# Kernel optimization log

Hardware: AMD Instinct MI355X
Metric: run time of the kernel (lower is better)

## Reference

```python
import jax, jax.numpy as jnp
import numpy as np

N, B, L, C, H = 16384, 16, 32, 256, 8
DH = C // H
K_STATIC = 16   # k_max for L=32 (L>20 -> min(16, L//2))
K_MIN = 8       # int(0.25*L)
LN_EPS = 1e-5


def _ln(x, g, b):
    m = x.mean(-1, keepdims=True)
    v = ((x - m) ** 2).mean(-1, keepdims=True)
    return (x - m) / jnp.sqrt(v + LN_EPS) * g + b


def setup_inputs() -> dict:
    key = jax.random.key(0)
    ks = jax.random.split(key, 12)
    s = 1.0 / np.sqrt(C)
    f32 = jnp.float32
    return {
        'vision_features': jax.random.normal(ks[0], (N, B, C), dtype=f32),
        'text_features': jax.random.normal(ks[1], (L, B, C), dtype=f32),
        'vp_w': jax.random.normal(ks[2], (C, C), dtype=f32) * s,
        'vp_b': jnp.zeros((C,), f32),
        'tp_w': jax.random.normal(ks[3], (C, C), dtype=f32) * s,
        'tp_b': jnp.zeros((C,), f32),
        'in_proj_w': jax.random.normal(ks[4], (3 * C, C), dtype=f32) * s,
        'in_proj_b': jnp.zeros((3 * C,), f32),
        'w1': jax.random.normal(ks[5], (C, C), dtype=f32) * s,
        'b1': jnp.zeros((C,), f32),
        'g1': jnp.ones((C,), f32),
        'be1': jnp.zeros((C,), f32),
        'w2': jax.random.normal(ks[6], (C // 2, C), dtype=f32) * s,
        'b2': jnp.zeros((C // 2,), f32),
        'g2': jnp.ones((C // 2,), f32),
        'be2': jnp.zeros((C // 2,), f32),
        'w3': jax.random.normal(ks[7], (1, C // 2), dtype=f32) * s,
        'b3': jnp.zeros((1,), f32),
        'k_weight': jnp.asarray(np.log(0.4 / 0.6), f32),
        'alpha_coarse': jnp.asarray(np.log(0.72 / 0.28), f32),
        'alpha_fine': jnp.asarray(np.log(0.82 / 0.18), f32),
    }


def reference(vision_features, text_features, vp_w, vp_b, tp_w, tp_b,
              in_proj_w, in_proj_b, w1, b1, g1, be1, w2, b2, g2, be2,
              w3, b3, k_weight, alpha_coarse, alpha_fine):
    # projections (torch Linear: y = x W^T + b)
    vision_proj = vision_features @ vp_w.T + vp_b  # [N,B,C]
    text_proj = text_features @ tp_w.T + tp_b      # [L,B,C]

    # nn.MultiheadAttention attention weights, averaged over heads
    qp = vision_proj @ in_proj_w[:C].T + in_proj_b[:C]
    kp = text_proj @ in_proj_w[C:2 * C].T + in_proj_b[C:2 * C]
    q = qp.reshape(N, B, H, DH)
    k = kp.reshape(L, B, H, DH)
    scores = jnp.einsum('nbhd,lbhd->bhnl', q, k) / np.sqrt(DH)
    attn = jax.nn.softmax(scores, axis=-1).mean(axis=1)  # [B,N,L]

    # data-dependent k_top per batch (unbiased variance over L, mean over N)
    mu = attn.mean(axis=-1, keepdims=True)
    var = ((attn - mu) ** 2).sum(axis=-1) / (L - 1)       # [B,N]
    attn_variance = var.mean(axis=1)                      # [B]
    k_ws = jax.nn.sigmoid(k_weight)
    ratio = jnp.clip(k_ws * (1.0 + attn_variance * 0.5), 0.25, 0.6)
    k_base = jnp.maximum(1, jnp.floor(L * ratio).astype(jnp.int32))
    k_top = jnp.maximum(K_MIN, jnp.minimum(jnp.minimum(K_STATIC, k_base), L))  # [B]

    # variable-k top-k via static K_STATIC + mask
    top = -jnp.sort(-attn, axis=-1)[..., :K_STATIC]       # [B,N,K]
    mask = jnp.arange(K_STATIC)[None, None, :] < k_top[:, None, None]
    logits = jnp.where(mask, top, -jnp.inf)
    w = jax.nn.softmax(logits, axis=-1)
    similarity_score = jnp.sum(jnp.where(mask, top * w, 0.0), axis=-1)  # [B,N]

    # importance MLP on raw vision features (dropout off at inference)
    h = jax.nn.relu(_ln(vision_features @ w1.T + b1, g1, be1))
    h = jax.nn.relu(_ln(h @ w2.T + b2, g2, be2))
    feature_importance = jax.nn.sigmoid(h @ w3.T + b3)[..., 0]  # [N,B]
    feature_importance = feature_importance.T                    # [B,N]

    def minmax(x):
        lo = x.min(axis=1, keepdims=True)
        rng = x.max(axis=1, keepdims=True) - lo
        return jnp.where(rng > 0, (x - lo) / rng, 0.0)

    sim_norm = minmax(similarity_score)
    imp_norm = minmax(feature_importance)

    alpha = (jax.nn.sigmoid(alpha_coarse) + jax.nn.sigmoid(alpha_fine)) / 2.0
    importance = alpha * sim_norm + (1.0 - alpha) * imp_norm  # [B,N]
    return importance.T  # [N,B]
```

## Files before the change

kernel.cpp:

```cpp
#include <hip/hip_runtime.h>
#include <hip/hip_bf16.h>

typedef _Float16 f16;
typedef _Float16 half8 __attribute__((ext_vector_type(8)));
typedef _Float16 half4 __attribute__((ext_vector_type(4)));
typedef float f32x4 __attribute__((ext_vector_type(4)));

typedef const __attribute__((address_space(1))) void gvoid;
typedef __attribute__((address_space(3))) void lvoid;
#define GLOAD16(src, dst) __builtin_amdgcn_global_load_lds((gvoid*)(src), (lvoid*)(dst), 16, 0, 0)

#define WQV_OFF   0u
#define WKT_OFF   262144u
#define KP_OFF    524288u
#define W2S_OFF   1048576u
#define SBIAS_OFF 3145728u
#define BQV_OFF   3162112u
#define BKT_OFF   3163136u
#define W1H_OFF   3164160u
#define W2H_OFF   3295232u
#define VARP_OFF  3360768u
#define SMM_OFF   3377280u
#define FMM_OFF   3377408u
#define CAND_OFF  3377664u
#define FI_OFF    12814848u
#define SIM_OFF   13863424u

__device__ __forceinline__ float sigm(float x) { return 1.f / (1.f + __expf(-x)); }
__device__ __forceinline__ unsigned fmap(float f) {
  unsigned u = __float_as_uint(f);
  return (u & 0x80000000u) ? ~u : (u | 0x80000000u);
}
__device__ __forceinline__ float funmap(unsigned u) {
  unsigned b = (u & 0x80000000u) ? (u & 0x7FFFFFFFu) : ~u;
  return __uint_as_float(b);
}
__device__ __forceinline__ unsigned fragoff(int o, int c) {
  int ot = o >> 4, ln = o & 15;
  int kc = c >> 6, mi = (c >> 5) & 1, kg = (c >> 3) & 3, h8 = c & 7;
  return (unsigned)((((ot * 4 + kc) * 2 + mi) << 10) + ((kg * 16 + ln) << 4) + h8 * 2);
}

__global__ void k_p1(const float* __restrict__ ipw, const float* __restrict__ ipb,
                     const float* __restrict__ vp_w, const float* __restrict__ vp_b,
                     const float* __restrict__ tp_w, const float* __restrict__ tp_b,
                     float* __restrict__ Wqv, float* __restrict__ Wkt,
                     float* __restrict__ bqv, float* __restrict__ bkt,
                     unsigned* __restrict__ simMM, unsigned* __restrict__ fiMM) {
  int tx = threadIdx.x, ty = threadIdx.y;
  int bz = blockIdx.z;
  if (bz == 2) {
    if (blockIdx.x || blockIdx.y) return;
    if (ty == 0 && tx < 16) {
      simMM[tx * 2] = 0xFFFFFFFFu; simMM[tx * 2 + 1] = 0u;
      fiMM[tx * 2] = 0xFFFFFFFFu;  fiMM[tx * 2 + 1] = 0u;
    }
    int j = ty * 16 + tx;
    float s1 = 0.f, s2 = 0.f;
    for (int k = 0; k < 256; ++k) {
      s1 += ipw[j * 256 + k] * vp_b[k];
      s2 += ipw[65536 + j * 256 + k] * tp_b[k];
    }
    bqv[j] = s1 + ipb[j];
    bkt[j] = s2 + ipb[256 + j];
    return;
  }
  const float* A = ipw + (bz ? 65536 : 0);
  const float* B = bz ? tp_w : vp_w;
  float* O = bz ? Wkt : Wqv;
  __shared__ float As[16][16], Bs[16][17];
  int row = blockIdx.y * 16 + ty, col = blockIdx.x * 16 + tx;
  float s = 0.f;
  for (int tt = 0; tt < 16; ++tt) {
    As[ty][tx] = A[row * 256 + tt * 16 + tx];
    Bs[ty][tx] = B[(tt * 16 + ty) * 256 + col];
    __syncthreads();
#pragma unroll
    for (int k = 0; k < 16; ++k) s += As[ty][k] * Bs[k][tx];
    __syncthreads();
  }
  O[row * 256 + col] = s;
}

__global__ void k_conv(const float* __restrict__ w1, const float* __restrict__ w2,
                       char* __restrict__ W1g, char* __restrict__ W2g) {
  int i = blockIdx.x * 256 + threadIdx.x;
  if (i < 65536) {
    int o = i >> 8, c = i & 255;
    *(f16*)(W1g + (c >> 6) * 32768 + o * 128 + (((c & 63) << 1) ^ ((o & 7) << 4))) = (f16)w1[i];
  } else if (i < 98304) {
    int i2 = i - 65536;
    int o = i2 >> 8, c = i2 & 255;
    *(f16*)(W2g + fragoff(o, c)) = (f16)w2[i2];
  }
}

__global__ void k_p2(const float* __restrict__ T, const float* __restrict__ Wkt,
                     const float* __restrict__ bkt, float* __restrict__ kp) {
  __shared__ float As[16][16], Ws[16][17];
  int tx = threadIdx.x, ty = threadIdx.y;
  int lb = blockIdx.y * 16 + ty;
  int i = blockIdx.x * 16 + tx;
  float s = 0.f;
  for (int tt = 0; tt < 16; ++tt) {
    As[ty][tx] = T[(size_t)lb * 256 + tt * 16 + tx];
    Ws[ty][tx] = Wkt[(size_t)(blockIdx.x * 16 + ty) * 256 + tt * 16 + tx];
    __syncthreads();
#pragma unroll
    for (int k = 0; k < 16; ++k) s += As[ty][k] * Ws[tx][k];
    __syncthreads();
  }
  kp[(size_t)lb * 256 + i] = s + bkt[i];
}

__global__ void k_p3(const float* __restrict__ kp, const float* __restrict__ Wqv,
                     const float* __restrict__ bqv, char* __restrict__ W2sg,
                     float* __restrict__ sbias) {
  const float SC = 0.17677669529663687f;
  int b = blockIdx.z, jt = blockIdx.y, ct = blockIdx.x;
  int ty = threadIdx.y, tx = threadIdx.x;
  int j2 = jt * 16 + ty, c = ct * 16 + tx;
  int h = j2 >> 5, l = j2 & 31;
  const float* kr = kp + (size_t)(l * 16 + b) * 256 + h * 32;
  const float* wq = Wqv + (size_t)h * 32 * 256 + c;
  float s = 0.f;
#pragma unroll
  for (int d = 0; d < 32; ++d) s += kr[d] * wq[(size_t)d * 256];
  *(f16*)(W2sg + (size_t)b * 131072 + (c >> 6) * 32768 + j2 * 128 +
          (((c & 63) << 1) ^ ((j2 & 7) << 4))) = (f16)(s * SC);
  if (ct == 0 && tx == 0) {
    float sb = 0.f;
#pragma unroll
    for (int d = 0; d < 32; ++d) sb += kr[d] * bqv[h * 32 + d];
    sbias[b * 256 + j2] = sb * SC;
  }
}

__global__ void __launch_bounds__(256, 4) k_main(
    const float* __restrict__ X, const char* __restrict__ W2sg,
    const float* __restrict__ sbias,
    const char* __restrict__ W1g, const char* __restrict__ W2g,
    const float* __restrict__ b1, const float* __restrict__ g1, const float* __restrict__ be1,
    const float* __restrict__ b2, const float* __restrict__ g2, const float* __restrict__ be2,
    const float* __restrict__ w3, const float* __restrict__ b3,
    float* __restrict__ cand, float* __restrict__ varpart, float* __restrict__ fi) {
  __shared__ __align__(16) char smem[40960];
  const int b = blockIdx.y;
  const int bx = blockIdx.x;
  const int n0 = bx * 64;
  const int t = threadIdx.x;
  const int w = t >> 6;
  const int lane = t & 63;
  const int ln = lane & 15, kg = lane >> 4;
  char* AT = smem;
  char* BT = smem + 8192;

  auto issueA = [&](int kt) {
    int row = t >> 2, cq = t & 3;
    const float* Xr = X + ((size_t)(n0 + row) * 16 + b) * 256 + kt * 64 + cq * 16;
    f32x4 a0 = *(const f32x4*)(Xr), a1 = *(const f32x4*)(Xr + 4);
    f32x4 a2 = *(const f32x4*)(Xr + 8), a3 = *(const f32x4*)(Xr + 12);
    half8 h0, h1;
#pragma unroll
    for (int i = 0; i < 4; ++i) {
      h0[i] = (f16)a0[i]; h0[4 + i] = (f16)a1[i];
      h1[i] = (f16)a2[i]; h1[4 + i] = (f16)a3[i];
    }
    unsigned sw = (unsigned)((row & 7) << 4);
    *(half8*)(AT + ((unsigned)(row * 128 + cq * 32) ^ sw)) = h0;
    *(half8*)(AT + ((unsigned)(row * 128 + cq * 32 + 16) ^ sw)) = h1;
  };

  if (blockIdx.z == 0) {
    const char* Wb = W2sg + (size_t)b * 131072;
    auto issueB = [&](int kt) {
      const char* src = Wb + kt * 32768 + w * 8192 + (lane << 4);
      char* dst = BT + w * 8192;
#pragma unroll
      for (int i = 0; i < 8; ++i) GLOAD16(src + i * 1024, dst + i * 1024);
    };

    f32x4 acc[4][4];
#pragma unroll
    for (int q = 0; q < 4; ++q)
#pragma unroll
      for (int ni = 0; ni < 4; ++ni)
#pragma unroll
        for (int i = 0; i < 4; ++i) acc[q][ni][i] = 0.f;

    issueA(0); issueB(0);
    __syncthreads();
#pragma unroll
    for (int kt = 0; kt < 4; ++kt) {
      half8 av[4][2], bv[4][2];
#pragma unroll
      for (int q = 0; q < 4; ++q) {
        int o = w * 64 + q * 16 + ln;
        unsigned sw = (unsigned)((o & 7) << 4);
#pragma unroll
        for (int mi = 0; mi < 2; ++mi)
          av[q][mi] = *(const half8*)(BT + o * 128 + ((unsigned)(mi * 64 + kg * 16) ^ sw));
      }
#pragma unroll
      for (int ni = 0; ni < 4; ++ni) {
        int n = ni * 16 + ln;
        unsigned sw = (unsigned)((n & 7) << 4);
#pragma unroll
        for (int mi = 0; mi < 2; ++mi)
          bv[ni][mi] = *(const half8*)(AT + n * 128 + ((unsigned)(mi * 64 + kg * 16) ^ sw));
      }
#pragma unroll
      for (int mi = 0; mi < 2; ++mi)
#pragma unroll
        for (int q = 0; q < 4; ++q)
#pragma unroll
          for (int ni = 0; ni < 4; ++ni)
            acc[q][ni] = __builtin_amdgcn_mfma_f32_16x16x32_f16(av[q][mi], bv[ni][mi], acc[q][ni], 0, 0, 0);
      __syncthreads();
      if (kt < 3) { issueA(kt + 1); issueB(kt + 1); __syncthreads(); }
    }

    {
      f32x4 sb[4];
#pragma unroll
      for (int q = 0; q < 4; ++q)
        sb[q] = *(const f32x4*)(sbias + b * 256 + (w * 4 + q) * 16 + kg * 4);
      float vm[4][2][4];
#pragma unroll
      for (int ni = 0; ni < 4; ++ni)
#pragma unroll
        for (int qq = 0; qq < 2; ++qq)
#pragma unroll
          for (int r = 0; r < 4; ++r) vm[ni][qq][r] = 0.f;
#pragma unroll
      for (int hh = 0; hh < 2; ++hh)
#pragma unroll
        for (int ni = 0; ni < 4; ++ni) {
          float x[2][4];
          float mx = -1e30f;
#pragma unroll
          for (int qq = 0; qq < 2; ++qq)
#pragma unroll
            for (int r = 0; r < 4; ++r) {
              x[qq][r] = acc[hh * 2 + qq][ni][r] + sb[hh * 2 + qq][r];
              mx = fmaxf(mx, x[qq][r]);
            }
          mx = fmaxf(mx, __shfl_xor(mx, 16, 64));
          mx = fmaxf(mx, __shfl_xor(mx, 32, 64));
          float S = 0.f;
#pragma unroll
          for (int qq = 0; qq < 2; ++qq)
#pragma unroll
            for (int r = 0; r < 4; ++r) { x[qq][r] = __expf(x[qq][r] - mx); S += x[qq][r]; }
          S += __shfl_xor(S, 16, 64);
          S += __shfl_xor(S, 32, 64);
          float inv = 0.125f / S;
#pragma unroll
          for (int qq = 0; qq < 2; ++qq)
#pragma unroll
            for (int r = 0; r < 4; ++r) vm[ni][qq][r] += x[qq][r] * inv;
        }
      float* slice = (float*)(smem + 8192) + w * 2048;
#pragma unroll
      for (int ni = 0; ni < 4; ++ni)
#pragma unroll
        for (int qq = 0; qq < 2; ++qq)
#pragma unroll
          for (int r = 0; r < 4; ++r)
            slice[(qq * 16 + kg * 4 + r) * 64 + ni * 16 + ln] = vm[ni][qq][r];
    }
    __syncthreads();

    if (w == 0) {
      const float* sl = (const float*)(smem + 8192);
      float v[32];
#pragma unroll
      for (int l = 0; l < 32; ++l)
        v[l] = sl[l * 64 + lane] + sl[2048 + l * 64 + lane] +
               sl[4096 + l * 64 + lane] + sl[6144 + l * 64 + lane];
      float s2 = 0.f;
#pragma unroll
      for (int l = 0; l < 32; ++l) s2 += v[l] * v[l];
      float vr = (s2 - (1.f / 32.f)) * (1.f / 31.f);
#pragma unroll
      for (int m = 1; m < 64; m <<= 1) vr += __shfl_xor(vr, m, 64);
      if (lane == 0) varpart[b * 256 + bx] = vr;
#pragma unroll
      for (int k = 2; k <= 32; k <<= 1) {
#pragma unroll
        for (int j = k >> 1; j > 0; j >>= 1) {
#pragma unroll
          for (int i = 0; i < 32; ++i) {
            int l = i ^ j;
            if (l > i) {
              float a = v[i], c = v[l];
              float hi = fmaxf(a, c), lo = fminf(a, c);
              bool up = ((i & k) == 0);
              v[i] = up ? hi : lo;
              v[l] = up ? lo : hi;
            }
          }
        }
      }
      float m0 = v[0], se = 0.f, te = 0.f;
      float cn[9];
#pragma unroll
      for (int i = 0; i < 16; ++i) {
        float e = __expf(v[i] - m0);
        se += e; te += v[i] * e;
        if (i >= 7) cn[i - 7] = te / se;
      }
#pragma unroll
      for (int i = 0; i < 9; ++i)
        cand[(size_t)i * 262144 + (size_t)b * 16384 + n0 + lane] = cn[i];
    }
    return;
  }

  char* H1 = smem;
  float* pS = (float*)(smem + 32768);
  float* pQ = (float*)(smem + 34048);
  float* pM = (float*)(smem + 35328);
  float* pR = (float*)(smem + 35584);
  auto issueB1 = [&](int kt) {
    const char* src = W1g + kt * 32768 + w * 8192 + (lane << 4);
    char* dst = BT + w * 8192;
#pragma unroll
    for (int i = 0; i < 8; ++i) GLOAD16(src + i * 1024, dst + i * 1024);
  };

  f32x4 acc[4][4];
#pragma unroll
  for (int q = 0; q < 4; ++q)
#pragma unroll
    for (int ni = 0; ni < 4; ++ni)
#pragma unroll
      for (int i = 0; i < 4; ++i) acc[q][ni][i] = 0.f;

  issueA(0); issueB1(0);
  __syncthreads();
#pragma unroll
  for (int kt = 0; kt < 4; ++kt) {
    half8 av[4][2], bv[4][2];
#pragma unroll
    for (int q = 0; q < 4; ++q) {
      int o = w * 64 + q * 16 + ln;
      unsigned sw = (unsigned)((o & 7) << 4);
#pragma unroll
      for (int mi = 0; mi < 2; ++mi)
        av[q][mi] = *(const half8*)(BT + o * 128 + ((unsigned)(mi * 64 + kg * 16) ^ sw));
    }
#pragma unroll
    for (int ni = 0; ni < 4; ++ni) {
      int n = ni * 16 + ln;
      unsigned sw = (unsigned)((n & 7) << 4);
#pragma unroll
      for (int mi = 0; mi < 2; ++mi)
        bv[ni][mi] = *(const half8*)(AT + n * 128 + ((unsigned)(mi * 64 + kg * 16) ^ sw));
    }
#pragma unroll
    for (int mi = 0; mi < 2; ++mi)
#pragma unroll
      for (int q = 0; q < 4; ++q)
#pragma unroll
        for (int ni = 0; ni < 4; ++ni)
          acc[q][ni] = __builtin_amdgcn_mfma_f32_16x16x32_f16(av[q][mi], bv[ni][mi], acc[q][ni], 0, 0, 0);
    __syncthreads();
    if (kt < 3) { issueA(kt + 1); issueB1(kt + 1); __syncthreads(); }
  }

  {
    f32x4 b1v[4];
#pragma unroll
    for (int q = 0; q < 4; ++q)
      b1v[q] = *(const f32x4*)(b1 + (w * 4 + q) * 16 + kg * 4);
#pragma unroll
    for (int ni = 0; ni < 4; ++ni) {
      float s = 0.f, qq = 0.f;
#pragma unroll
      for (int q = 0; q < 4; ++q)
#pragma unroll
        for (int r = 0; r < 4; ++r) {
          float v = acc[q][ni][r] + b1v[q][r];
          acc[q][ni][r] = v;
          s += v; qq += v * v;
        }
      s += __shfl_xor(s, 16, 64); s += __shfl_xor(s, 32, 64);
      qq += __shfl_xor(qq, 16, 64); qq += __shfl_xor(qq, 32, 64);
      if (kg == 0) { int n = ni * 16 + ln; pS[n * 5 + w] = s; pQ[n * 5 + w] = qq; }
    }
  }
  __syncthreads();
  if (t < 64) {
    float s = pS[t * 5 + 0] + pS[t * 5 + 1] + pS[t * 5 + 2] + pS[t * 5 + 3];
    float q = pQ[t * 5 + 0] + pQ[t * 5 + 1] + pQ[t * 5 + 2] + pQ[t * 5 + 3];
    float mean = s * (1.f / 256.f);
    float var = q * (1.f / 256.f) - mean * mean;
    pM[t] = mean;
    pR[t] = rsqrtf(var + 1e-5f);
  }
  __syncthreads();

  {
    f32x4 g1v[4], e1v[4];
#pragma unroll
    for (int q = 0; q < 4; ++q) {
      g1v[q] = *(const f32x4*)(g1 + (w * 4 + q) * 16 + kg * 4);
      e1v[q] = *(const f32x4*)(be1 + (w * 4 + q) * 16 + kg * 4);
    }
#pragma unroll
    for (int ni = 0; ni < 4; ++ni) {
      int n = ni * 16 + ln;
      float mean = pM[n], rstd = pR[n];
      unsigned sw = (unsigned)((n & 7) << 4);
#pragma unroll
      for (int q = 0; q < 4; ++q) {
        half4 hv;
#pragma unroll
        for (int r = 0; r < 4; ++r) {
          float y = (acc[q][ni][r] - mean) * rstd * g1v[q][r] + e1v[q][r];
          hv[r] = (f16)fmaxf(y, 0.f);
        }
        *(half4*)(H1 + ((unsigned)(n * 512 + (w * 4 + q) * 32 + kg * 8) ^ sw)) = hv;
      }
    }
  }
  __syncthreads();

  f32x4 acc2[2][4];
#pragma unroll
  for (int oi = 0; oi < 2; ++oi)
#pragma unroll
    for (int ni = 0; ni < 4; ++ni)
#pragma unroll
      for (int i = 0; i < 4; ++i) acc2[oi][ni][i] = 0.f;
#pragma unroll
  for (int kt = 0; kt < 4; ++kt) {
    half8 a2[2][2], bv[4][2];
#pragma unroll
    for (int oi = 0; oi < 2; ++oi)
#pragma unroll
      for (int mi = 0; mi < 2; ++mi)
        a2[oi][mi] = *(const half8*)(W2g + ((((w * 2 + oi) * 4 + kt) * 2 + mi) << 10) + (lane << 4));
#pragma unroll
    for (int ni = 0; ni < 4; ++ni) {
      int n = ni * 16 + ln;
      unsigned sw = (unsigned)((n & 7) << 4);
#pragma unroll
      for (int mi = 0; mi < 2; ++mi)
        bv[ni][mi] = *(const half8*)(H1 + n * 512 + kt * 128 + ((unsigned)(mi * 64 + kg * 16) ^ sw));
    }
#pragma unroll
    for (int mi = 0; mi < 2; ++mi)
#pragma unroll
      for (int oi = 0; oi < 2; ++oi)
#pragma unroll
        for (int ni = 0; ni < 4; ++ni)
          acc2[oi][ni] = __builtin_amdgcn_mfma_f32_16x16x32_f16(a2[oi][mi], bv[ni][mi], acc2[oi][ni], 0, 0, 0);
  }

  {
    f32x4 b2v[2], g2v[2], e2v[2], w3v[2];
#pragma unroll
    for (int oi = 0; oi < 2; ++oi) {
      b2v[oi] = *(const f32x4*)(b2 + (w * 2 + oi) * 16 + kg * 4);
      g2v[oi] = *(const f32x4*)(g2 + (w * 2 + oi) * 16 + kg * 4);
      e2v[oi] = *(const f32x4*)(be2 + (w * 2 + oi) * 16 + kg * 4);
      w3v[oi] = *(const f32x4*)(w3 + (w * 2 + oi) * 16 + kg * 4);
    }
    __syncthreads();
#pragma unroll
    for (int ni = 0; ni < 4; ++ni) {
      float s = 0.f, q = 0.f;
#pragma unroll
      for (int oi = 0; oi < 2; ++oi)
#pragma unroll
        for (int r = 0; r < 4; ++r) {
          float v = acc2[oi][ni][r] + b2v[oi][r];
          acc2[oi][ni][r] = v;
          s += v; q += v * v;
        }
      s += __shfl_xor(s, 16, 64); s += __shfl_xor(s, 32, 64);
      q += __shfl_xor(q, 16, 64); q += __shfl_xor(q, 32, 64);
      if (kg == 0) { int n = ni * 16 + ln; pS[n * 5 + w] = s; pQ[n * 5 + w] = q; }
    }
    __syncthreads();
    if (t < 64) {
      float s = pS[t * 5 + 0] + pS[t * 5 + 1] + pS[t * 5 + 2] + pS[t * 5 + 3];
      float q = pQ[t * 5 + 0] + pQ[t * 5 + 1] + pQ[t * 5 + 2] + pQ[t * 5 + 3];
      float mean = s * (1.f / 128.f);
      float var = q * (1.f / 128.f) - mean * mean;
      pM[t] = mean;
      pR[t] = rsqrtf(var + 1e-5f);
    }
    __syncthreads();
#pragma unroll
    for (int ni = 0; ni < 4; ++ni) {
      int n = ni * 16 + ln;
      float mean = pM[n], rstd = pR[n];
      float a3 = 0.f;
#pragma unroll
      for (int oi = 0; oi < 2; ++oi)
#pragma unroll
        for (int r = 0; r < 4; ++r) {
          float y = (acc2[oi][ni][r] - mean) * rstd * g2v[oi][r] + e2v[oi][r];
          a3 += fmaxf(y, 0.f) * w3v[oi][r];
        }
      a3 += __shfl_xor(a3, 16, 64);
      a3 += __shfl_xor(a3, 32, 64);
      if (kg == 0) pS[n * 5 + w] = a3;
    }
    __syncthreads();
    if (t < 64) {
      float z = pS[t * 5 + 0] + pS[t * 5 + 1] + pS[t * 5 + 2] + pS[t * 5 + 3] + b3[0];
      fi[(size_t)b * 16384 + n0 + t] = sigm(z);
    }
  }
}

__global__ void __launch_bounds__(256) k_g4(
    const float* __restrict__ cand, const float* __restrict__ fi,
    const float* __restrict__ varpart, const float* __restrict__ kw,
    float* __restrict__ sim, unsigned* __restrict__ simMM, unsigned* __restrict__ fiMM) {
  __shared__ float red[4][4];
  __shared__ int kS;
  int b = blockIdx.x >> 6;
  if (threadIdx.x < 64) {
    float s = 0.f;
#pragma unroll
    for (int i = 0; i < 4; ++i) s += varpart[b * 256 + threadIdx.x + i * 64];
#pragma unroll
    for (int m = 1; m < 64; m <<= 1) s += __shfl_xor(s, m, 64);
    if (threadIdx.x == 0) {
      float var = s * (1.f / 16384.f);
      float kws = sigm(kw[0]);
      float ratio = fminf(fmaxf(kws * (1.f + var * 0.5f), 0.25f), 0.6f);
      int kb = (int)floorf(32.f * ratio);
      if (kb < 1) kb = 1;
      int kt = kb < 16 ? kb : 16;
      if (kt < 8) kt = 8;
      kS = kt;
    }
  }
  __syncthreads();
  int k = kS;
  int n = (blockIdx.x & 63) * 256 + threadIdx.x;
  size_t idx = (size_t)b * 16384 + n;
  float sv = cand[(size_t)(k - 8) * 262144 + idx];
  sim[idx] = sv;
  float fv = fi[idx];
  float sn = sv, sx = sv, fn = fv, fx = fv;
#pragma unroll
  for (int m = 1; m < 64; m <<= 1) {
    sn = fminf(sn, __shfl_xor(sn, m, 64));
    sx = fmaxf(sx, __shfl_xor(sx, m, 64));
    fn = fminf(fn, __shfl_xor(fn, m, 64));
    fx = fmaxf(fx, __shfl_xor(fx, m, 64));
  }
  int wv = threadIdx.x >> 6;
  if ((threadIdx.x & 63) == 0) { red[0][wv] = sn; red[1][wv] = sx; red[2][wv] = fn; red[3][wv] = fx; }
  __syncthreads();
  if (threadIdx.x == 0) {
    float a = red[0][0], c = red[1][0], d = red[2][0], e = red[3][0];
#pragma unroll
    for (int i = 1; i < 4; ++i) {
      a = fminf(a, red[0][i]); c = fmaxf(c, red[1][i]);
      d = fminf(d, red[2][i]); e = fmaxf(e, red[3][i]);
    }
    atomicMin(&simMM[b * 2 + 0], fmap(a));
    atomicMax(&simMM[b * 2 + 1], fmap(c));
    atomicMin(&fiMM[b * 2 + 0], fmap(d));
    atomicMax(&fiMM[b * 2 + 1], fmap(e));
  }
}

__global__ void __launch_bounds__(256) k_g5(
    const float* __restrict__ sim, const float* __restrict__ fi,
    const unsigned* __restrict__ simMM, const unsigned* __restrict__ fiMM,
    const float* __restrict__ ac, const float* __restrict__ af,
    float* __restrict__ out) {
  __shared__ float ls[256][17], lf[256][17];
  __shared__ float sMin[16], sInv[16], fMin[16], fInv[16];
  int t = threadIdx.x;
  int n0 = blockIdx.x * 256;
  if (t < 16) {
    float lo = funmap(simMM[t * 2]), hi = funmap(simMM[t * 2 + 1]);
    float r = hi - lo;
    sMin[t] = lo; sInv[t] = (r > 0.f) ? 1.f / r : 0.f;
    lo = funmap(fiMM[t * 2]); hi = funmap(fiMM[t * 2 + 1]);
    r = hi - lo;
    fMin[t] = lo; fInv[t] = (r > 0.f) ? 1.f / r : 0.f;
  }
#pragma unroll
  for (int i = 0; i < 16; ++i) {
    ls[t][i] = sim[(size_t)i * 16384 + n0 + t];
    lf[t][i] = fi[(size_t)i * 16384 + n0 + t];
  }
  __syncthreads();
  float alpha = 0.5f * (sigm(ac[0]) + sigm(af[0]));
  float o[16];
#pragma unroll
  for (int b = 0; b < 16; ++b) {
    float s = (ls[t][b] - sMin[b]) * sInv[b];
    float f = (lf[t][b] - fMin[b]) * fInv[b];
    o[b] = alpha * s + (1.f - alpha) * f;
  }
  float* op = out + (size_t)(n0 + t) * 16;
#pragma unroll
  for (int i = 0; i < 4; ++i) {
    f32x4 v;
    v[0] = o[i * 4]; v[1] = o[i * 4 + 1]; v[2] = o[i * 4 + 2]; v[3] = o[i * 4 + 3];
    *(f32x4*)(op + i * 4) = v;
  }
}

extern "C" void kernel_launch(void* const* d_in, const int* in_sizes, int n_in,
                              void* d_out, int out_size, void* d_ws, size_t ws_size,
                              hipStream_t stream) {
  const float* X    = (const float*)d_in[0];
  const float* T    = (const float*)d_in[1];
  const float* vp_w = (const float*)d_in[2];
  const float* vp_b = (const float*)d_in[3];
  const float* tp_w = (const float*)d_in[4];
  const float* tp_b = (const float*)d_in[5];
  const float* ipw  = (const float*)d_in[6];
  const float* ipb  = (const float*)d_in[7];
  const float* w1   = (const float*)d_in[8];
  const float* b1   = (const float*)d_in[9];
  const float* g1   = (const float*)d_in[10];
  const float* be1  = (const float*)d_in[11];
  const float* w2   = (const float*)d_in[12];
  const float* b2   = (const float*)d_in[13];
  const float* g2   = (const float*)d_in[14];
  const float* be2  = (const float*)d_in[15];
  const float* w3   = (const float*)d_in[16];
  const float* b3   = (const float*)d_in[17];
  const float* kw   = (const float*)d_in[18];
  const float* ac   = (const float*)d_in[19];
  const float* af   = (const float*)d_in[20];
  char* ws = (char*)d_ws;
  float* Wqv = (float*)(ws + WQV_OFF);
  float* Wkt = (float*)(ws + WKT_OFF);
  float* kp = (float*)(ws + KP_OFF);
  char* W2sg = ws + W2S_OFF;
  float* sbias = (float*)(ws + SBIAS_OFF);
  float* bqv = (float*)(ws + BQV_OFF);
  float* bkt = (float*)(ws + BKT_OFF);
  char* W1g = ws + W1H_OFF;
  char* W2g = ws + W2H_OFF;
  float* varpart = (float*)(ws + VARP_OFF);
  unsigned* simMM = (unsigned*)(ws + SMM_OFF);
  unsigned* fiMM = (unsigned*)(ws + FMM_OFF);
  float* cand = (float*)(ws + CAND_OFF);
  float* fi = (float*)(ws + FI_OFF);
  float* sim = (float*)(ws + SIM_OFF);
  float* out = (float*)d_out;

  k_p1<<<dim3(16, 16, 3), dim3(16, 16), 0, stream>>>(ipw, ipb, vp_w, vp_b, tp_w, tp_b,
                                                     Wqv, Wkt, bqv, bkt, simMM, fiMM);
  k_conv<<<384, 256, 0, stream>>>(w1, w2, W1g, W2g);
  k_p2<<<dim3(16, 32), dim3(16, 16), 0, stream>>>(T, Wkt, bkt, kp);
  k_p3<<<dim3(16, 16, 16), dim3(16, 16), 0, stream>>>(kp, Wqv, bqv, W2sg, sbias);
  k_main<<<dim3(256, 16, 2), 256, 0, stream>>>(X, W2sg, sbias, W1g, W2g,
                                               b1, g1, be1, b2, g2, be2, w3, b3,
                                               cand, varpart, fi);
  k_g4<<<1024, 256, 0, stream>>>(cand, fi, varpart, kw, sim, simMM, fiMM);
  k_g5<<<64, 256, 0, stream>>>(sim, fi, simMM, fiMM, ac, af, out);
}
```

Baseline: 257.4 us.

## Merge attention and MLP branches of k_main to share one staged X tile

The two blockIdx.z branches of k_main, which each loaded and converted the same 64-row X tile, become one block that stages the full fp16 X tile in shared memory once. The block then runs the attention-score GEMM and the importance-MLP GEMM in sequence, reusing both the X tile and the weight buffer, and writes the first-layer activations back over the X region. This halves the global X reads and the f32-to-f16 conversion work. In exchange, shared memory grows to about 67KB, launch bounds drop to 2 blocks per SM, and each block does serial work with less parallelism across blocks.

```diff
diff --git a/kernel.cpp b/kernel.cpp
--- a/kernel.cpp
+++ b/kernel.cpp
@@ -136,7 +136,7 @@
   }
 }
 
-__global__ void __launch_bounds__(256, 4) k_main(
+__global__ void __launch_bounds__(256, 2) k_main(
     const float* __restrict__ X, const char* __restrict__ W2sg,
     const float* __restrict__ sbias,
     const char* __restrict__ W1g, const char* __restrict__ W2g,
@@ -144,7 +144,7 @@
     const float* __restrict__ b2, const float* __restrict__ g2, const float* __restrict__ be2,
     const float* __restrict__ w3, const float* __restrict__ b3,
     float* __restrict__ cand, float* __restrict__ varpart, float* __restrict__ fi) {
-  __shared__ __align__(16) char smem[40960];
+  __shared__ __align__(16) char smem[68608];
   const int b = blockIdx.y;
   const int bx = blockIdx.x;
   const int n0 = bx * 64;
@@ -152,221 +152,192 @@
   const int w = t >> 6;
   const int lane = t & 63;
   const int ln = lane & 15, kg = lane >> 4;
-  char* AT = smem;
-  char* BT = smem + 8192;
-
-  auto issueA = [&](int kt) {
+  char* XT = smem;
+  char* WB = smem + 32768;
+  float* pS = (float*)(smem + 65536);
+  float* pQ = (float*)(smem + 66816);
+  float* pM = (float*)(smem + 68096);
+  float* pR = (float*)(smem + 68352);
+
+  {
     int row = t >> 2, cq = t & 3;
-    const float* Xr = X + ((size_t)(n0 + row) * 16 + b) * 256 + kt * 64 + cq * 16;
-    f32x4 a0 = *(const f32x4*)(Xr), a1 = *(const f32x4*)(Xr + 4);
-    f32x4 a2 = *(const f32x4*)(Xr + 8), a3 = *(const f32x4*)(Xr + 12);
-    half8 h0, h1;
-#pragma unroll
-    for (int i = 0; i < 4; ++i) {
-      h0[i] = (f16)a0[i]; h0[4 + i] = (f16)a1[i];
-      h1[i] = (f16)a2[i]; h1[4 + i] = (f16)a3[i];
-    }
+    const float* Xr = X + ((size_t)(n0 + row) * 16 + b) * 256;
     unsigned sw = (unsigned)((row & 7) << 4);
-    *(half8*)(AT + ((unsigned)(row * 128 + cq * 32) ^ sw)) = h0;
-    *(half8*)(AT + ((unsigned)(row * 128 + cq * 32 + 16) ^ sw)) = h1;
+#pragma unroll
+    for (int kt = 0; kt < 4; ++kt) {
+      f32x4 a0 = *(const f32x4*)(Xr + kt * 64 + cq * 16);
+      f32x4 a1 = *(const f32x4*)(Xr + kt * 64 + cq * 16 + 4);
+      f32x4 a2 = *(const f32x4*)(Xr + kt * 64 + cq * 16 + 8);
+      f32x4 a3 = *(const f32x4*)(Xr + kt * 64 + cq * 16 + 12);
+      half8 h0, h1;
+#pragma unroll
+      for (int i = 0; i < 4; ++i) {
+        h0[i] = (f16)a0[i]; h0[4 + i] = (f16)a1[i];
+        h1[i] = (f16)a2[i]; h1[4 + i] = (f16)a3[i];
+      }
+      unsigned base = (unsigned)(row * 512 + kt * 128 + cq * 32);
+      *(half8*)(XT + ((base) ^ sw)) = h0;
+      *(half8*)(XT + ((base + 16) ^ sw)) = h1;
+    }
+  }
+
+  auto issueW = [&](const char* Wimg, int kt) {
+    const char* src = Wimg + kt * 32768 + w * 8192 + (lane << 4);
+    char* dst = WB + w * 8192;
+#pragma unroll
+    for (int i = 0; i < 8; ++i) GLOAD16(src + i * 1024, dst + i * 1024);
   };
 
-  if (blockIdx.z == 0) {
-    const char* Wb = W2sg + (size_t)b * 131072;
-    auto issueB = [&](int kt) {
-      const char* src = Wb + kt * 32768 + w * 8192 + (lane << 4);
-      char* dst = BT + w * 8192;
-#pragma unroll
-      for (int i = 0; i < 8; ++i) GLOAD16(src + i * 1024, dst + i * 1024);
-    };
-
-    f32x4 acc[4][4];
+  f32x4 acc[4][4];
+  auto zeroAcc = [&]() {
 #pragma unroll
     for (int q = 0; q < 4; ++q)
 #pragma unroll
       for (int ni = 0; ni < 4; ++ni)
 #pragma unroll
         for (int i = 0; i < 4; ++i) acc[q][ni][i] = 0.f;
-
-    issueA(0); issueB(0);
-    __syncthreads();
-#pragma unroll
-    for (int kt = 0; kt < 4; ++kt) {
-      half8 av[4][2], bv[4][2];
-#pragma unroll
-      for (int q = 0; q < 4; ++q) {
-        int o = w * 64 + q * 16 + ln;
-        unsigned sw = (unsigned)((o & 7) << 4);
-#pragma unroll
-        for (int mi = 0; mi < 2; ++mi)
-          av[q][mi] = *(const half8*)(BT + o * 128 + ((unsigned)(mi * 64 + kg * 16) ^ sw));
+  };
+  auto gemm_kt = [&](int kt) {
+    half8 av[4][2], bv[4][2];
+#pragma unroll
+    for (int q = 0; q < 4; ++q) {
+      int o = w * 64 + q * 16 + ln;
+      unsigned sw = (unsigned)((o & 7) << 4);
+#pragma unroll
+      for (int mi = 0; mi < 2; ++mi)
+        av[q][mi] = *(const half8*)(WB + o * 128 + ((unsigned)(mi * 64 + kg * 16) ^ sw));
+    }
+#pragma unroll
+    for (int ni = 0; ni < 4; ++ni) {
+      int n = ni * 16 + ln;
+      unsigned sw = (unsigned)((n & 7) << 4);
+#pragma unroll
+      for (int mi = 0; mi < 2; ++mi)
+        bv[ni][mi] = *(const half8*)(XT + n * 512 + kt * 128 + ((unsigned)(mi * 64 + kg * 16) ^ sw));
+    }
+#pragma unroll
+    for (int mi = 0; mi < 2; ++mi)
+#pragma unroll
+      for (int q = 0; q < 4; ++q)
+#pragma unroll
+        for (int ni = 0; ni < 4; ++ni)
+          acc[q][ni] = __builtin_amdgcn_mfma_f32_16x16x32_f16(av[q][mi], bv[ni][mi], acc[q][ni], 0, 0, 0);
+  };
+
+  zeroAcc();
+  issueW(W2sg + (size_t)b * 131072, 0);
+  __syncthreads();
+#pragma unroll
+  for (int kt = 0; kt < 4; ++kt) {
+    gemm_kt(kt);
+    __syncthreads();
+    if (kt < 3) { issueW(W2sg + (size_t)b * 131072, kt + 1); __syncthreads(); }
+  }
+
+  {
+    f32x4 sb[4];
+#pragma unroll
+    for (int q = 0; q < 4; ++q)
+      sb[q] = *(const f32x4*)(sbias + b * 256 + (w * 4 + q) * 16 + kg * 4);
+    float vm[4][2][4];
+#pragma unroll
+    for (int ni = 0; ni < 4; ++ni)
+#pragma unroll
+      for (int qq = 0; qq < 2; ++qq)
+#pragma unroll
+        for (int r = 0; r < 4; ++r) vm[ni][qq][r] = 0.f;
+#pragma unroll
+    for (int hh = 0; hh < 2; ++hh)
+#pragma unroll
+      for (int ni = 0; ni < 4; ++ni) {
+        float x[2][4];
+        float mx = -1e30f;
+#pragma unroll
+        for (int qq = 0; qq < 2; ++qq)
+#pragma unroll
+          for (int r = 0; r < 4; ++r) {
+            x[qq][r] = acc[hh * 2 + qq][ni][r] + sb[hh * 2 + qq][r];
+            mx = fmaxf(mx, x[qq][r]);
+          }
+        mx = fmaxf(mx, __shfl_xor(mx, 16, 64));
+        mx = fmaxf(mx, __shfl_xor(mx, 32, 64));
+        float S = 0.f;
+#pragma unroll
+        for (int qq = 0; qq < 2; ++qq)
+#pragma unroll
+          for (int r = 0; r < 4; ++r) { x[qq][r] = __expf(x[qq][r] - mx); S += x[qq][r]; }
+        S += __shfl_xor(S, 16, 64);
+        S += __shfl_xor(S, 32, 64);
+        float inv = 0.125f / S;
+#pragma unroll
+        for (int qq = 0; qq < 2; ++qq)
+#pragma unroll
+          for (int r = 0; r < 4; ++r) vm[ni][qq][r] += x[qq][r] * inv;
       }
-#pragma unroll
-      for (int ni = 0; ni < 4; ++ni) {
-        int n = ni * 16 + ln;
-        unsigned sw = (unsigned)((n & 7) << 4);
-#pragma unroll
-        for (int mi = 0; mi < 2; ++mi)
-          bv[ni][mi] = *(const half8*)(AT + n * 128 + ((unsigned)(mi * 64 + kg * 16) ^ sw));
-      }
-#pragma unroll
-      for (int mi = 0; mi < 2; ++mi)
-#pragma unroll
-        for (int q = 0; q < 4; ++q)
-#pragma unroll
-          for (int ni = 0; ni < 4; ++ni)
-            acc[q][ni] = __builtin_amdgcn_mfma_f32_16x16x32_f16(av[q][mi], bv[ni][mi], acc[q][ni], 0, 0, 0);
-      __syncthreads();
-      if (kt < 3) { issueA(kt + 1); issueB(kt + 1); __syncthreads(); }
-    }
-
-    {
-      f32x4 sb[4];
-#pragma unroll
-      for (int q = 0; q < 4; ++q)
-        sb[q] = *(const f32x4*)(sbias + b * 256 + (w * 4 + q) * 16 + kg * 4);
-      float vm[4][2][4];
-#pragma unroll
-      for (int ni = 0; ni < 4; ++ni)
-#pragma unroll
-        for (int qq = 0; qq < 2; ++qq)
-#pragma unroll
-          for (int r = 0; r < 4; ++r) vm[ni][qq][r] = 0.f;
-#pragma unroll
-      for (int hh = 0; hh < 2; ++hh)
-#pragma unroll
-        for (int ni = 0; ni < 4; ++ni) {
-          float x[2][4];
-          float mx = -1e30f;
-#pragma unroll
-          for (int qq = 0; qq < 2; ++qq)
-#pragma unroll
-            for (int r = 0; r < 4; ++r) {
-              x[qq][r] = acc[hh * 2 + qq][ni][r] + sb[hh * 2 + qq][r];
-              mx = fmaxf(mx, x[qq][r]);
-            }
-          mx = fmaxf(mx, __shfl_xor(mx, 16, 64));
-          mx = fmaxf(mx, __shfl_xor(mx, 32, 64));
-          float S = 0.f;
-#pragma unroll
-          for (int qq = 0; qq < 2; ++qq)
-#pragma unroll
-            for (int r = 0; r < 4; ++r) { x[qq][r] = __expf(x[qq][r] - mx); S += x[qq][r]; }
-          S += __shfl_xor(S, 16, 64);
-          S += __shfl_xor(S, 32, 64);
-          float inv = 0.125f / S;
-#pragma unroll
-          for (int qq = 0; qq < 2; ++qq)
-#pragma unroll
-            for (int r = 0; r < 4; ++r) vm[ni][qq][r] += x[qq][r] * inv;
-        }
-      float* slice = (float*)(smem + 8192) + w * 2048;
-#pragma unroll
-      for (int ni = 0; ni < 4; ++ni)
-#pragma unroll
-        for (int qq = 0; qq < 2; ++qq)
-#pragma unroll
-          for (int r = 0; r < 4; ++r)
-            slice[(qq * 16 + kg * 4 + r) * 64 + ni * 16 + ln] = vm[ni][qq][r];
-    }
-    __syncthreads();
-
-    if (w == 0) {
-      const float* sl = (const float*)(smem + 8192);
-      float v[32];
-#pragma unroll
-      for (int l = 0; l < 32; ++l)
-        v[l] = sl[l * 64 + lane] + sl[2048 + l * 64 + lane] +
-               sl[4096 + l * 64 + lane] + sl[6144 + l * 64 + lane];
-      float s2 = 0.f;
-#pragma unroll
-      for (int l = 0; l < 32; ++l) s2 += v[l] * v[l];
-      float vr = (s2 - (1.f / 32.f)) * (1.f / 31.f);
-#pragma unroll
-      for (int m = 1; m < 64; m <<= 1) vr += __shfl_xor(vr, m, 64);
-      if (lane == 0) varpart[b * 256 + bx] = vr;
-#pragma unroll
-      for (int k = 2; k <= 32; k <<= 1) {
-#pragma unroll
-        for (int j = k >> 1; j > 0; j >>= 1) {
-#pragma unroll
-          for (int i = 0; i < 32; ++i) {
-            int l = i ^ j;
-            if (l > i) {
-              float a = v[i], c = v[l];
-              float hi = fmaxf(a, c), lo = fminf(a, c);
-              bool up = ((i & k) == 0);
-              v[i] = up ? hi : lo;
-              v[l] = up ? lo : hi;
-            }
+    float* slice = (float*)WB + w * 2048;
+#pragma unroll
+    for (int ni = 0; ni < 4; ++ni)
+#pragma unroll
+      for (int qq = 0; qq < 2; ++qq)
+#pragma unroll
+        for (int r = 0; r < 4; ++r)
+          slice[(qq * 16 + kg * 4 + r) * 64 + ni * 16 + ln] = vm[ni][qq][r];
+  }
+  __syncthreads();
+
+  if (w == 0) {
+    const float* sl = (const float*)WB;
+    float v[32];
+#pragma unroll
+    for (int l = 0; l < 32; ++l)
+      v[l] = sl[l * 64 + lane] + sl[2048 + l * 64 + lane] +
+             sl[4096 + l * 64 + lane] + sl[6144 + l * 64 + lane];
+    float s2 = 0.f;
+#pragma unroll
+    for (int l = 0; l < 32; ++l) s2 += v[l] * v[l];
+    float vr = (s2 - (1.f / 32.f)) * (1.f / 31.f);
+#pragma unroll
+    for (int m = 1; m < 64; m <<= 1) vr += __shfl_xor(vr, m, 64);
+    if (lane == 0) varpart[b * 256 + bx] = vr;
+#pragma unroll
+    for (int k = 2; k <= 32; k <<= 1) {
+#pragma unroll
+      for (int j = k >> 1; j > 0; j >>= 1) {
+#pragma unroll
+        for (int i = 0; i < 32; ++i) {
+          int l = i ^ j;
+          if (l > i) {
+            float a = v[i], c = v[l];
+            float hi = fmaxf(a, c), lo = fminf(a, c);
+            bool up = ((i & k) == 0);
+            v[i] = up ? hi : lo;
+            v[l] = up ? lo : hi;
           }
         }
       }
-      float m0 = v[0], se = 0.f, te = 0.f;
-      float cn[9];
-#pragma unroll
-      for (int i = 0; i < 16; ++i) {
-        float e = __expf(v[i] - m0);
-        se += e; te += v[i] * e;
-        if (i >= 7) cn[i - 7] = te / se;
-      }
-#pragma unroll
-      for (int i = 0; i < 9; ++i)
-        cand[(size_t)i * 262144 + (size_t)b * 16384 + n0 + lane] = cn[i];
-    }
-    return;
-  }
-
-  char* H1 = smem;
-  float* pS = (float*)(smem + 32768);
-  float* pQ = (float*)(smem + 34048);
-  float* pM = (float*)(smem + 35328);
-  float* pR = (float*)(smem + 35584);
-  auto issueB1 = [&](int kt) {
-    const char* src = W1g + kt * 32768 + w * 8192 + (lane << 4);
-    char* dst = BT + w * 8192;
-#pragma unroll
-    for (int i = 0; i < 8; ++i) GLOAD16(src + i * 1024, dst + i * 1024);
-  };
-
-  f32x4 acc[4][4];
-#pragma unroll
-  for (int q = 0; q < 4; ++q)
-#pragma unroll
-    for (int ni = 0; ni < 4; ++ni)
-#pragma unroll
-      for (int i = 0; i < 4; ++i) acc[q][ni][i] = 0.f;
-
-  issueA(0); issueB1(0);
+    }
+    float m0 = v[0], se = 0.f, te = 0.f;
+    float cn[9];
+#pragma unroll
+    for (int i = 0; i < 16; ++i) {
+      float e = __expf(v[i] - m0);
+      se += e; te += v[i] * e;
+      if (i >= 7) cn[i - 7] = te / se;
+    }
+#pragma unroll
+    for (int i = 0; i < 9; ++i)
+      cand[(size_t)i * 262144 + (size_t)b * 16384 + n0 + lane] = cn[i];
+  }
+  __syncthreads();
+
+  zeroAcc();
+  issueW(W1g, 0);
   __syncthreads();
 #pragma unroll
   for (int kt = 0; kt < 4; ++kt) {
-    half8 av[4][2], bv[4][2];
-#pragma unroll
-    for (int q = 0; q < 4; ++q) {
-      int o = w * 64 + q * 16 + ln;
-      unsigned sw = (unsigned)((o & 7) << 4);
-#pragma unroll
-      for (int mi = 0; mi < 2; ++mi)
-        av[q][mi] = *(const half8*)(BT + o * 128 + ((unsigned)(mi * 64 + kg * 16) ^ sw));
-    }
-#pragma unroll
-    for (int ni = 0; ni < 4; ++ni) {
-      int n = ni * 16 + ln;
-      unsigned sw = (unsigned)((n & 7) << 4);
-#pragma unroll
-      for (int mi = 0; mi < 2; ++mi)
-        bv[ni][mi] = *(const half8*)(AT + n * 128 + ((unsigned)(mi * 64 + kg * 16) ^ sw));
-    }
-#pragma unroll
-    for (int mi = 0; mi < 2; ++mi)
-#pragma unroll
-      for (int q = 0; q < 4; ++q)
-#pragma unroll
-        for (int ni = 0; ni < 4; ++ni)
-          acc[q][ni] = __builtin_amdgcn_mfma_f32_16x16x32_f16(av[q][mi], bv[ni][mi], acc[q][ni], 0, 0, 0);
-    __syncthreads();
-    if (kt < 3) { issueA(kt + 1); issueB1(kt + 1); __syncthreads(); }
+    gemm_kt(kt);
+    __syncthreads();
+    if (kt < 3) { issueW(W1g, kt + 1); __syncthreads(); }
   }
 
   {
@@ -421,7 +392,7 @@
           float y = (acc[q][ni][r] - mean) * rstd * g1v[q][r] + e1v[q][r];
           hv[r] = (f16)fmaxf(y, 0.f);
         }
-        *(half4*)(H1 + ((unsigned)(n * 512 + (w * 4 + q) * 32 + kg * 8) ^ sw)) = hv;
+        *(half4*)(XT + ((unsigned)(n * 512 + (w * 4 + q) * 32 + kg * 8) ^ sw)) = hv;
       }
     }
   }
@@ -448,7 +419,7 @@
       unsigned sw = (unsigned)((n & 7) << 4);
 #pragma unroll
       for (int mi = 0; mi < 2; ++mi)
-        bv[ni][mi] = *(const half8*)(H1 + n * 512 + kt * 128 + ((unsigned)(mi * 64 + kg * 16) ^ sw));
+        bv[ni][mi] = *(const half8*)(XT + n * 512 + kt * 128 + ((unsigned)(mi * 64 + kg * 16) ^ sw));
     }
 #pragma unroll
     for (int mi = 0; mi < 2; ++mi)
@@ -661,9 +632,9 @@
   k_conv<<<384, 256, 0, stream>>>(w1, w2, W1g, W2g);
   k_p2<<<dim3(16, 32), dim3(16, 16), 0, stream>>>(T, Wkt, bkt, kp);
   k_p3<<<dim3(16, 16, 16), dim3(16, 16), 0, stream>>>(kp, Wqv, bqv, W2sg, sbias);
-  k_main<<<dim3(256, 16, 2), 256, 0, stream>>>(X, W2sg, sbias, W1g, W2g,
-                                               b1, g1, be1, b2, g2, be2, w3, b3,
-                                               cand, varpart, fi);
+  k_main<<<dim3(256, 16), 256, 0, stream>>>(X, W2sg, sbias, W1g, W2g,
+                                            b1, g1, be1, b2, g2, be2, w3, b3,
+                                            cand, varpart, fi);
   k_g4<<<1024, 256, 0, stream>>>(cand, fi, varpart, kw, sim, simMM, fiMM);
   k_g5<<<64, 256, 0, stream>>>(sim, fi, simMM, fiMM, ac, af, out);
 }
```

After: 251.3 us, median of 2. 1.02x faster.
